# Optimization experiments

Hardware: AMD Instinct MI355X
Metric: run time of the kernel (lower is better)

## Reference

```python
import jax, jax.numpy as jnp
import numpy as np

N = 4096
FIN = 512
HID = 256
NCLS = 2
NE = 131072

def _glorot(key, fan_in, fan_out):
    r = np.sqrt(6.0 / (fan_in + fan_out))
    return jax.random.uniform(key, (fan_in, fan_out), jnp.float32, -r, r)

def setup_inputs() -> dict:
    key = jax.random.key(0)
    ks = jax.random.split(key, 16)
    X = jax.random.normal(ks[0], (N, FIN), jnp.float32)
    adj_rows = jax.random.randint(ks[1], (NE,), 0, N, jnp.int32)
    adj_cols = jax.random.randint(ks[2], (NE,), 0, N, jnp.int32)
    adj_vals = jax.random.uniform(ks[3], (NE,), jnp.float32)
    W_shared = _glorot(ks[4], FIN, HID)
    W_iv = _glorot(ks[5], HID, HID)
    W_c = _glorot(ks[6], HID, HID)
    W_r = _glorot(ks[7], HID, HID)
    Wg_iv = _glorot(ks[8], HID, HID)
    Wg_c = _glorot(ks[9], HID, HID)
    Wg_r = _glorot(ks[10], HID, HID)
    lin_W = _glorot(ks[11], 2 * HID, NCLS)
    lin_b = jnp.zeros((NCLS,), jnp.float32)
    return {"X": X, "adj_rows": adj_rows, "adj_cols": adj_cols, "adj_vals": adj_vals,
            "W_shared": W_shared, "W_iv": W_iv, "W_c": W_c, "W_r": W_r,
            "Wg_iv": Wg_iv, "Wg_c": Wg_c, "Wg_r": Wg_r, "lin_W": lin_W, "lin_b": lin_b}

def _spmm(rows, cols, vals, m):
    # sparse.mm(adj, m): out[i] = sum_{e: rows[e]==i} vals[e] * m[cols[e]]
    return jax.ops.segment_sum(vals[:, None] * m[cols], rows, num_segments=N)

def _gcn(x, rows, cols, vals, W):
    # dropout is identity in eval mode
    return jax.nn.relu(_spmm(rows, cols, vals, x @ W))

def _graphite(x, r1, r2, W):
    h = x @ W
    return jax.nn.relu(r1 @ (r1.T @ h) + r2 @ (r2.T @ h))

def reference(X, adj_rows, adj_cols, adj_vals, W_shared, W_iv, W_c, W_r, Wg_iv, Wg_c, Wg_r, lin_W, lin_b):
    h = _gcn(X, adj_rows, adj_cols, adj_vals, W_shared)
    z_iv0 = _gcn(h, adj_rows, adj_cols, adj_vals, W_iv)
    z_c0 = _gcn(h, adj_rows, adj_cols, adj_vals, W_c)
    z_r0 = _gcn(h, adj_rows, adj_cols, adj_vals, W_r)
    z_iv_rec0 = z_iv0 @ z_iv0.T
    z_c_rec0 = z_c0 @ z_c0.T
    z_r_rec0 = z_r0 @ z_r0.T
    A_dense = jnp.zeros((N, N), jnp.float32).at[adj_rows, adj_cols].add(adj_vals)
    z_iv = _graphite(z_iv0, A_dense, jax.nn.sigmoid(z_iv_rec0), Wg_iv)
    z_c = _graphite(z_c0, A_dense, jax.nn.sigmoid(z_c_rec0), Wg_c)
    z_r = _graphite(z_r0, A_dense, jax.nn.sigmoid(z_r_rec0), Wg_r)
    z_iv_rec = z_iv @ z_iv.T
    z_c_rec = z_c @ z_c.T
    z_r_rec = z_r @ z_r.T
    concat = jnp.concatenate([z_iv, z_c], axis=1)
    pred_T = jax.nn.log_softmax(concat @ lin_W + lin_b, axis=1)
    mi_total_loss = jnp.array(0.0, jnp.float32)
    return (z_iv, z_iv_rec, z_c, z_c_rec, z_r, z_r_rec, mi_total_loss, pred_T)
```

## Files before the change

kernel.cpp:

```cpp
#include <hip/hip_runtime.h>

#define Nn   4096
#define FINd 512
#define HIDd 256
#define NEd  131072

typedef unsigned short u16;
typedef __bf16 bf16x8 __attribute__((ext_vector_type(8)));
typedef float floatx4 __attribute__((ext_vector_type(4)));

__device__ __forceinline__ float bf2f(u16 u) {
  union { unsigned int i; float f; } v; v.i = ((unsigned int)u) << 16; return v.f;
}
__device__ __forceinline__ u16 f2bf(float f) {
  union { unsigned int i; float f; } v; v.f = f;
  unsigned int x = v.i;
  return (u16)((x + 0x7FFFu + ((x >> 16) & 1u)) >> 16);
}

#define GLDS(gp, lp) __builtin_amdgcn_global_load_lds( \
    (__attribute__((address_space(1))) unsigned int*)(void*)(gp), \
    (__attribute__((address_space(3))) unsigned int*)(lp), 16, 0, 0)

__global__ __launch_bounds__(256) void hist_priv_k(const int* __restrict__ rows,
                                                   const int* __restrict__ cols,
                                                   int* __restrict__ slabs) {
  __shared__ int cnt[8192];
  const int t = threadIdx.x;
  for (int i = t; i < 8192; i += 256) cnt[i] = 0;
  __syncthreads();
  int base = blockIdx.x * 4096;
  for (int i = t; i < 4096; i += 256) {
    int e = base + i;
    atomicAdd(&cnt[rows[e]], 1);
    atomicAdd(&cnt[4096 + cols[e]], 1);
  }
  __syncthreads();
  int* out = slabs + blockIdx.x * 8192;
  for (int i = t; i < 8192; i += 256) out[i] = cnt[i];
}

__global__ __launch_bounds__(1024) void scan2_k(const unsigned int* __restrict__ X,
                                                const int* __restrict__ slabs,
                                                int* __restrict__ rp, int* __restrict__ cp,
                                                int* __restrict__ rfill, int* __restrict__ cfill,
                                                int* __restrict__ flag) {
  __shared__ int part[1024];
  __shared__ int dcnt;
  const int t = threadIdx.x;
  if (t == 0) dcnt = 0;
  __syncthreads();
  int local = 0;
  for (int i = t; i < 4096; i += 1024) {
    unsigned e = (X[i] >> 7) & 0xFFu;
    if (e >= 100u && e <= 140u) local++;
  }
  if (local) atomicAdd(&dcnt, local);
  int base = t * 8, s = 0, loc[8];
  int csum[8];
#pragma unroll
  for (int j = 0; j < 8; ++j) csum[j] = 0;
  for (int sl = 0; sl < 32; ++sl) {
    const int* sp = slabs + sl * 8192 + base;
#pragma unroll
    for (int j = 0; j < 8; ++j) csum[j] += sp[j];
  }
#pragma unroll
  for (int j = 0; j < 8; ++j) { loc[j] = s; s += csum[j]; }
  part[t] = s;
  __syncthreads();
  if (t == 0) *flag = (dcnt > 2458) ? 1 : 0;
  for (int off = 1; off < 1024; off <<= 1) {
    int v = (t >= off) ? part[t - off] : 0;
    __syncthreads();
    part[t] += v;
    __syncthreads();
  }
  int excl = (t == 0) ? 0 : part[t - 1];
  int rtot = part[511];
  if (t < 512) {
#pragma unroll
    for (int j = 0; j < 8; ++j) rp[base + j] = excl + loc[j];
    if (t == 511) rp[4096] = rtot;
  } else {
    int cb = base - 4096;
    int ex2 = excl - rtot;
#pragma unroll
    for (int j = 0; j < 8; ++j) cp[cb + j] = ex2 + loc[j];
    if (t == 1023) cp[4096] = part[1023] - rtot;
  }
  for (int i = t; i < 4096; i += 1024) { rfill[i] = 0; cfill[i] = 0; }
}

__global__ __launch_bounds__(256) void setup2_k(const void* __restrict__ X,
                                                const void* __restrict__ Wsh,
                                                const void* __restrict__ W0, const void* __restrict__ W1,
                                                const void* __restrict__ W2, const void* __restrict__ G0,
                                                const void* __restrict__ G1, const void* __restrict__ G2,
                                                const void* __restrict__ linW, const void* __restrict__ linb,
                                                const int* __restrict__ rows, const int* __restrict__ cols,
                                                const void* __restrict__ vals,
                                                const int* __restrict__ rp, const int* __restrict__ cp,
                                                int* __restrict__ rfill, int* __restrict__ cfill,
                                                int2* __restrict__ rpack, int2* __restrict__ cpack,
                                                u16* __restrict__ Xb, u16* __restrict__ WshT,
                                                u16* __restrict__ WTb, u16* __restrict__ WgTb,
                                                float* __restrict__ linWf, float* __restrict__ linbf,
                                                const int* __restrict__ flag) {
  int fl = *flag;
  int bx = blockIdx.x;
  if (bx >= 10245) {
    int e = (bx - 10245) * 256 + threadIdx.x;
    if (e >= NEd) return;
    float v = fl ? bf2f(((const u16*)vals)[e]) : ((const float*)vals)[e];
    int r = rows[e], c = cols[e];
    int p1 = rp[r] + atomicAdd(&rfill[r], 1);
    rpack[p1] = make_int2(c, __float_as_int(v));
    int p2 = cp[c] + atomicAdd(&cfill[c], 1);
    cpack[p2] = make_int2(r, __float_as_int(v));
    return;
  }
  int i = bx * 256 + threadIdx.x;
  if (i < 2097152) {
    Xb[i] = fl ? ((const u16*)X)[i] : f2bf(((const float*)X)[i]);
    return;
  }
  int i2 = i - 2097152;
  if (i2 < 131072) {
    int r = i2 >> 8, c = i2 & 255;
    u16 v = fl ? ((const u16*)Wsh)[i2] : f2bf(((const float*)Wsh)[i2]);
    WshT[c * 512 + r] = v;
    return;
  }
  int i3 = i2 - 131072;
  if (i3 < 393216) {
    int w = i3 >> 16, j = i3 & 65535;
    int r = j >> 8, c = j & 255;
    const void* src = (w == 0) ? W0 : (w == 1) ? W1 : (w == 2) ? W2
                     : (w == 3) ? G0 : (w == 4) ? G1 : G2;
    u16 v = fl ? ((const u16*)src)[j] : f2bf(((const float*)src)[j]);
    u16* dst = (w < 3) ? (WTb + w * 65536) : (WgTb + (w - 3) * 65536);
    dst[c * 256 + r] = v;
    return;
  }
  int i4 = i3 - 393216;
  if (i4 < 1024) { linWf[i4] = fl ? bf2f(((const u16*)linW)[i4]) : ((const float*)linW)[i4]; return; }
  if (i4 < 1026) { int k = i4 - 1024; linbf[k] = fl ? bf2f(((const u16*)linb)[k]) : ((const float*)linb)[k]; }
}

struct SPP {
  const int* ptr; const int2* ep;
  const u16* m[3]; u16* ob[3]; unsigned long long oo[3];
};
__global__ __launch_bounds__(256) void spmm_mb_k(SPP s, const float* __restrict__ part,
                                                 void* __restrict__ outbase, int mode,
                                                 const int* __restrict__ flag) {
  const int b = blockIdx.y;
  int gid = blockIdx.x * 256 + threadIdx.x;
  int row = gid >> 6, lane = gid & 63, f = lane << 2;
  int beg = s.ptr[row], end = s.ptr[row + 1];
  const u16* m = s.m[b];
  float ax = 0.f, ay = 0.f, az = 0.f, aw = 0.f;
  int e = beg;
  for (; e + 1 < end; e += 2) {
    int2 c0 = s.ep[e];
    int2 c1 = s.ep[e + 1];
    ushort4 m0 = *(const ushort4*)(m + (size_t)c0.x * HIDd + f);
    ushort4 m1 = *(const ushort4*)(m + (size_t)c1.x * HIDd + f);
    float v0 = __int_as_float(c0.y), v1 = __int_as_float(c1.y);
    ax = fmaf(v1, bf2f(m1.x), fmaf(v0, bf2f(m0.x), ax));
    ay = fmaf(v1, bf2f(m1.y), fmaf(v0, bf2f(m0.y), ay));
    az = fmaf(v1, bf2f(m1.z), fmaf(v0, bf2f(m0.z), az));
    aw = fmaf(v1, bf2f(m1.w), fmaf(v0, bf2f(m0.w), aw));
  }
  if (e < end) {
    int2 cv = s.ep[e];
    float v = __int_as_float(cv.y);
    ushort4 mv = *(const ushort4*)(m + (size_t)cv.x * HIDd + f);
    ax = fmaf(v, bf2f(mv.x), ax);
    ay = fmaf(v, bf2f(mv.y), ay);
    az = fmaf(v, bf2f(mv.z), az);
    aw = fmaf(v, bf2f(mv.w), aw);
  }
  size_t o = (size_t)row * HIDd + f;
  if (mode == 2) {
    const float* pb = part + (size_t)b * 1048576 + o;
    float4 p0 = *(const float4*)(pb);
    float4 p1 = *(const float4*)(pb + 3145728);
    float4 p2 = *(const float4*)(pb + 2 * 3145728);
    float4 p3 = *(const float4*)(pb + 3 * 3145728);
    ax += p0.x + p1.x + p2.x + p3.x;
    ay += p0.y + p1.y + p2.y + p3.y;
    az += p0.z + p1.z + p2.z + p3.z;
    aw += p0.w + p1.w + p2.w + p3.w;
    ax = fmaxf(ax, 0.f); ay = fmaxf(ay, 0.f);
    az = fmaxf(az, 0.f); aw = fmaxf(aw, 0.f);
    ushort4 o4 = { f2bf(ax), f2bf(ay), f2bf(az), f2bf(aw) };
    *(ushort4*)(s.ob[b] + o) = o4;
    if (*flag) *(ushort4*)((u16*)outbase + s.oo[b] + o) = o4;
    else       *(float4*)((float*)outbase + s.oo[b] + o) = make_float4(ax, ay, az, aw);
  } else {
    if (mode == 0) {
      ax = fmaxf(ax, 0.f); ay = fmaxf(ay, 0.f);
      az = fmaxf(az, 0.f); aw = fmaxf(aw, 0.f);
    }
    ushort4 o4 = { f2bf(ax), f2bf(ay), f2bf(az), f2bf(aw) };
    *(ushort4*)(s.ob[b] + o) = o4;
  }
}

__global__ __launch_bounds__(256) void redt_k(const float* __restrict__ part,
                                              u16* __restrict__ tT) {
  int i = (blockIdx.x * 256 + threadIdx.x) * 4;
  float4 s0 = *(const float4*)(part + i);
  float4 s1 = *(const float4*)(part + i + 3145728);
  float4 s2 = *(const float4*)(part + i + 2 * 3145728);
  float4 s3 = *(const float4*)(part + i + 3 * 3145728);
  ushort4 o = { f2bf(s0.x + s1.x + s2.x + s3.x), f2bf(s0.y + s1.y + s2.y + s3.y),
                f2bf(s0.z + s1.z + s2.z + s3.z), f2bf(s0.w + s1.w + s2.w + s3.w) };
  *(ushort4*)(tT + i) = o;
}

struct TQ {
  const u16* Ap[3]; const u16* Bp[3]; unsigned long long c0[3];
  int tallA, K, N, kspan;
  const int* cp; const int2* cep;
  const u16* hp[3]; u16* ub[3];
};

__global__ __launch_bounds__(512) void tall_spmmu_k(TQ P, float* __restrict__ partf) {
  __shared__ __align__(16) u16 smem[24576];
  const int b = blockIdx.z;
  const int bx = blockIdx.x;
  if (bx >= 128) {
    int gid = (bx - 128) * 512 + threadIdx.x;
    int row = gid >> 6, lane = gid & 63, f = lane << 2;
    int beg = P.cp[row], end = P.cp[row + 1];
    const u16* m = P.hp[b];
    float ax = 0.f, ay = 0.f, az = 0.f, aw = 0.f;
    int e = beg;
    for (; e + 1 < end; e += 2) {
      int2 c0 = P.cep[e];
      int2 c1 = P.cep[e + 1];
      ushort4 m0 = *(const ushort4*)(m + (size_t)c0.x * HIDd + f);
      ushort4 m1 = *(const ushort4*)(m + (size_t)c1.x * HIDd + f);
      float v0 = __int_as_float(c0.y), v1 = __int_as_float(c1.y);
      ax = fmaf(v1, bf2f(m1.x), fmaf(v0, bf2f(m0.x), ax));
      ay = fmaf(v1, bf2f(m1.y), fmaf(v0, bf2f(m0.y), ay));
      az = fmaf(v1, bf2f(m1.z), fmaf(v0, bf2f(m0.z), az));
      aw = fmaf(v1, bf2f(m1.w), fmaf(v0, bf2f(m0.w), aw));
    }
    if (e < end) {
      int2 cv = P.cep[e];
      float v = __int_as_float(cv.y);
      ushort4 mv = *(const ushort4*)(m + (size_t)cv.x * HIDd + f);
      ax = fmaf(v, bf2f(mv.x), ax);
      ay = fmaf(v, bf2f(mv.y), ay);
      az = fmaf(v, bf2f(mv.z), az);
      aw = fmaf(v, bf2f(mv.w), aw);
    }
    size_t o = (size_t)row * HIDd + f;
    ushort4 o4 = { f2bf(ax), f2bf(ay), f2bf(az), f2bf(aw) };
    *(ushort4*)(P.ub[b] + o) = o4;
    return;
  }
  const u16* A = P.Ap[b];
  const u16* B = P.Bp[b];
  const int K = P.K, N = P.N, tallA = P.tallA;
  const int stripe = bx & 31, ks = bx >> 5;
  const int tid = threadIdx.x, w = tid >> 6, lane = tid & 63;
  const int lr = lane >> 3, cc = lane & 7;
  const int scol = (cc ^ lr) << 3;
  u16* As = smem;
  u16* Bs = smem + (tallA ? 16384 : 8192);
  int wrow, wcol;
  if (tallA) { wrow = (w >> 1) * 64; wcol = (w & 1) * 64; }
  else       { wrow = (w >> 2) * 64; wcol = (w & 3) * 64; }
  const int row0 = tallA ? 0 : stripe * 128;
  const int col0 = tallA ? stripe * 128 : 0;
  const int na = tallA ? 4 : 2;
  const int nb = tallA ? 2 : 4;
  floatx4 acc[4][4] = {};
  int aoff[4], boff[4];
#pragma unroll
  for (int i = 0; i < 4; ++i) {
    int m = wrow + i * 16 + (lane & 15);
    aoff[i] = m * 64 + (((lane >> 4) << 3) ^ ((m & 7) << 3));
    int n = wcol + i * 16 + (lane & 15);
    boff[i] = n * 64 + (((lane >> 4) << 3) ^ ((n & 7) << 3));
  }
  const int kbeg = ks * P.kspan, kend = kbeg + P.kspan;
  for (int k0 = kbeg; k0 < kend; k0 += 64) {
#pragma unroll
    for (int t = 0; t < 4; ++t) {
      if (t < na) {
        int ch = na * w + t;
        GLDS(A + (size_t)(row0 + 8 * ch + lr) * K + k0 + scol, As + ch * 512);
      }
      if (t < nb) {
        int ch = nb * w + t;
        GLDS(B + (size_t)(col0 + 8 * ch + lr) * K + k0 + scol, Bs + ch * 512);
      }
    }
    __syncthreads();
#pragma unroll
    for (int kk = 0; kk < 2; ++kk) {
      bf16x8 af[4], bfr[4];
#pragma unroll
      for (int i = 0; i < 4; ++i) {
        af[i]  = *(const bf16x8*)(As + (aoff[i] ^ (kk << 5)));
        bfr[i] = *(const bf16x8*)(Bs + (boff[i] ^ (kk << 5)));
      }
#pragma unroll
      for (int i = 0; i < 4; ++i)
#pragma unroll
        for (int j = 0; j < 4; ++j)
          acc[i][j] = __builtin_amdgcn_mfma_f32_16x16x32_bf16(af[i], bfr[j], acc[i][j], 0, 0, 0);
    }
    __syncthreads();
  }
  const int l15 = lane & 15, q4 = (lane >> 4) << 2;
  float* C = partf + P.c0[b] + (size_t)ks * 3145728;
  const int cbase = col0 + wcol + l15;
#pragma unroll
  for (int i = 0; i < 4; ++i)
#pragma unroll
    for (int r = 0; r < 4; ++r) {
      size_t rb = (size_t)(row0 + wrow + i * 16 + q4 + r) * N + cbase;
#pragma unroll
      for (int j = 0; j < 4; ++j) C[rb + j * 16] = acc[i][j][r];
    }
}

struct Job {
  const u16* A; const u16* B;
  const float* F1; const float* F2;
  unsigned long long c0, c1, pstride;
  int M, N, K, mode, xt, ntiles, nks, kspan, sym;
};
struct Jobs { Job j[6]; };

__global__ __launch_bounds__(256) void gemm_mega(Jobs P, void* __restrict__ WSv,
                                                 void* __restrict__ OutO,
                                                 const int* __restrict__ flag) {
  __shared__ __align__(16) u16 smem[17408];
  u16* As = smem;
  u16* Bs = smem + 8192;
  u16* Ts = smem;
  const Job jb = P.j[blockIdx.z];
  const unsigned tile = blockIdx.x;
  if ((int)tile >= jb.ntiles * jb.nks) return;
  if (jb.mode == 6) {
    int i = tile * 256 + threadIdx.x;
    const float* lw = jb.F1;
    float a0 = jb.F2[0], a1 = jb.F2[1];
    for (int f = 0; f < HIDd; ++f) {
      float zv = bf2f(jb.A[(size_t)i * HIDd + f]);
      a0 = fmaf(zv, lw[2 * f + 0], a0);
      a1 = fmaf(zv, lw[2 * f + 1], a1);
    }
    for (int f = 0; f < HIDd; ++f) {
      float zv = bf2f(jb.B[(size_t)i * HIDd + f]);
      a0 = fmaf(zv, lw[2 * (HIDd + f) + 0], a0);
      a1 = fmaf(zv, lw[2 * (HIDd + f) + 1], a1);
    }
    float mx = fmaxf(a0, a1);
    float lse = mx + logf(expf(a0 - mx) + expf(a1 - mx));
    float p0 = a0 - lse, p1 = a1 - lse;
    if (*flag) {
      u16* ob = (u16*)OutO;
      ob[jb.c0 + 2 * i + 0] = f2bf(p0);
      ob[jb.c0 + 2 * i + 1] = f2bf(p1);
      if (i == 0) ob[jb.c1] = 0;
    } else {
      float* ob = (float*)OutO;
      ob[jb.c0 + 2 * i + 0] = p0;
      ob[jb.c0 + 2 * i + 1] = p1;
      if (i == 0) ob[jb.c1] = 0.f;
    }
    return;
  }
  const unsigned ks = tile / (unsigned)jb.ntiles;
  const unsigned t2 = tile - ks * jb.ntiles;
  unsigned ty, tx;
  if (jb.sym) {
    unsigned rem = t2, rowlen = jb.xt; ty = 0;
    while (rem >= rowlen) { rem -= rowlen; --rowlen; ++ty; }
    tx = ty + rem;
  } else {
    ty = t2 / (unsigned)jb.xt;
    tx = t2 - ty * jb.xt;
  }
  const int K = jb.K, N = jb.N;
  const int row0 = ty * 128, col0 = tx * 128;
  const int tid = threadIdx.x;
  const int w = tid >> 6, lane = tid & 63;
  const int wr = (w >> 1) * 64, wc = (w & 1) * 64;
  const int lr = lane >> 3, cc = lane & 7;
  const int scol = (cc ^ lr) << 3;
  floatx4 acc[4][4] = {};
  int aoff[4], boff[4];
#pragma unroll
  for (int i = 0; i < 4; ++i) {
    int m = wr + i * 16 + (lane & 15);
    aoff[i] = m * 64 + ((((lane >> 4) << 3)) ^ ((m & 7) << 3));
    int n = wc + i * 16 + (lane & 15);
    boff[i] = n * 64 + ((((lane >> 4) << 3)) ^ ((n & 7) << 3));
  }
  const u16* A = jb.A;
  const u16* B = jb.B;
  const int kbeg = ks * jb.kspan, kend = kbeg + jb.kspan;
  for (int k0 = kbeg; k0 < kend; k0 += 64) {
#pragma unroll
    for (int t = 0; t < 4; ++t) {
      int ch = 4 * w + t;
      GLDS(A + (size_t)(row0 + 8 * ch + lr) * K + k0 + scol, As + ch * 512);
      GLDS(B + (size_t)(col0 + 8 * ch + lr) * K + k0 + scol, Bs + ch * 512);
    }
    __syncthreads();
#pragma unroll
    for (int kk = 0; kk < 2; ++kk) {
      bf16x8 af[4], bfr[4];
#pragma unroll
      for (int i = 0; i < 4; ++i) {
        af[i]  = *(const bf16x8*)(As + (aoff[i] ^ (kk << 5)));
        bfr[i] = *(const bf16x8*)(Bs + (boff[i] ^ (kk << 5)));
      }
#pragma unroll
      for (int i = 0; i < 4; ++i)
#pragma unroll
        for (int j = 0; j < 4; ++j)
          acc[i][j] = __builtin_amdgcn_mfma_f32_16x16x32_bf16(af[i], bfr[j], acc[i][j], 0, 0, 0);
    }
    __syncthreads();
  }

  const int l15 = lane & 15, q4 = (lane >> 4) << 2;
  const int cb = col0 + wc + l15;
  const int mode = jb.mode;
  if (mode == 0 || mode == 1) {
    u16* C = ((mode == 1) ? (u16*)OutO : (u16*)WSv) + jb.c0;
#pragma unroll
    for (int i = 0; i < 4; ++i)
#pragma unroll
      for (int r = 0; r < 4; ++r) {
        int lrow = wr + i * 16 + q4 + r;
        size_t rb = (size_t)(row0 + lrow) * N + cb;
#pragma unroll
        for (int j = 0; j < 4; ++j) {
          float v = acc[i][j][r];
          if (mode == 1) v = 1.f / (1.f + __expf(-v));
          u16 vb = f2bf(v);
          C[rb + j * 16] = vb;
          if (jb.sym) Ts[(wc + j * 16 + l15) * 136 + lrow] = vb;
        }
      }
    if (jb.sym && tx != ty) {
      __syncthreads();
      int rr = tid >> 1, hf = (tid & 1) << 6;
      size_t rb2 = (size_t)(col0 + rr) * N + row0 + hf;
#pragma unroll
      for (int k = 0; k < 8; ++k)
        *(uint4*)(C + rb2 + k * 8) = *(const uint4*)(Ts + rr * 136 + hf + k * 8);
    }
  } else if (mode == 4) {
    u16* C  = (u16*)WSv + jb.c0;
    u16* CT = (u16*)WSv + jb.c1;
    const int M = jb.M;
#pragma unroll
    for (int i = 0; i < 4; ++i)
#pragma unroll
      for (int r = 0; r < 4; ++r) {
        int gr = row0 + wr + i * 16 + q4 + r;
#pragma unroll
        for (int j = 0; j < 4; ++j) {
          u16 v = f2bf(acc[i][j][r]);
          int gc = cb + j * 16;
          C[(size_t)gr * N + gc] = v;
          CT[(size_t)gc * M + gr] = v;
        }
      }
  } else {
    if (*flag) {
      u16* C = (u16*)OutO + jb.c0;
#pragma unroll
      for (int i = 0; i < 4; ++i)
#pragma unroll
        for (int r = 0; r < 4; ++r) {
          int lrow = wr + i * 16 + q4 + r;
          size_t rb = (size_t)(row0 + lrow) * N + cb;
#pragma unroll
          for (int j = 0; j < 4; ++j) {
            u16 vb = f2bf(acc[i][j][r]);
            C[rb + j * 16] = vb;
            if (jb.sym) Ts[(wc + j * 16 + l15) * 136 + lrow] = vb;
          }
        }
      if (jb.sym && tx != ty) {
        __syncthreads();
        int rr = tid >> 1, hf = (tid & 1) << 6;
        size_t rb2 = (size_t)(col0 + rr) * N + row0 + hf;
#pragma unroll
        for (int k = 0; k < 8; ++k)
          *(uint4*)(C + rb2 + k * 8) = *(const uint4*)(Ts + rr * 136 + hf + k * 8);
      }
    } else {
      float* C = (float*)OutO + jb.c0;
#pragma unroll
      for (int i = 0; i < 4; ++i)
#pragma unroll
        for (int r = 0; r < 4; ++r) {
          int gr = row0 + wr + i * 16 + q4 + r;
          size_t rb = (size_t)gr * N + cb;
#pragma unroll
          for (int j = 0; j < 4; ++j) C[rb + j * 16] = acc[i][j][r];
        }
      if (jb.sym && tx != ty) {
        float* Tf = (float*)smem;
        const int whalf = w & 1;
#pragma unroll
        for (int half = 0; half < 2; ++half) {
          __syncthreads();
          if (whalf == half) {
#pragma unroll
            for (int i = 0; i < 4; ++i)
#pragma unroll
              for (int j = 0; j < 4; ++j) {
                int cl = j * 16 + l15;
#pragma unroll
                for (int r = 0; r < 4; ++r)
                  Tf[cl * 132 + wr + i * 16 + q4 + r] = acc[i][j][r];
              }
          }
          __syncthreads();
          int cl = tid >> 2, chf = (tid & 3) << 5;
          size_t rb2 = (size_t)(col0 + half * 64 + cl) * N + row0 + chf;
          const float* src = Tf + cl * 132 + chf;
#pragma unroll
          for (int k = 0; k < 8; ++k)
            *(float4*)(C + rb2 + k * 4) = *(const float4*)(src + k * 4);
        }
      }
    }
  }
}

extern "C" void kernel_launch(void* const* d_in, const int* in_sizes, int n_in,
                              void* d_out, int out_size, void* d_ws, size_t ws_size,
                              hipStream_t stream) {
  const void* X    = d_in[0];
  const int*  rows = (const int*)d_in[1];
  const int*  cols = (const int*)d_in[2];
  const void* vals = d_in[3];
  const void* Wsh  = d_in[4];

  char* W = (char*)d_ws;
  u16*  Xb    = (u16*)(W + 0);
  u16*  WshT  = (u16*)(W + 4194304);
  u16*  WTb   = (u16*)(W + 4456448);
  u16*  WgTb  = (u16*)(W + 4849664);
  int*  rp    = (int*)(W + 5242880);
  int*  cp    = (int*)(W + 5275648);
  int*  rfill = (int*)(W + 5308416);
  int*  cfill = (int*)(W + 5324800);
  int2* rpack = (int2*)(W + 5341184);
  int2* cpack = (int2*)(W + 6389760);
  float* linWf = (float*)(W + 7438336);
  float* linbf = (float*)(W + 7442432);
  int*  flag  = (int*)(W + 7442560);
  u16*  hb    = (u16*)(W + 8388608);
  u16*  tmpb[3] = { (u16*)(W + 10485760), (u16*)(W + 12582912), (u16*)(W + 14680064) };
  u16*  z0b[3]  = { (u16*)(W + 16777216), (u16*)(W + 18874368), (u16*)(W + 20971520) };
  u16*  hpb[3]  = { (u16*)(W + 23068672), (u16*)(W + 25165824), (u16*)(W + 27262976) };
  u16*  hpT[3]  = { (u16*)(W + 29360128), (u16*)(W + 31457280), (u16*)(W + 33554432) };
  u16*  tTb     = (u16*)(W + 35651584);
  u16*  zbb[3]  = { (u16*)(W + 41943040), (u16*)(W + 44040192), (u16*)(W + 46137344) };
  u16*  ubb[3]  = { (u16*)(W + 48234496), (u16*)(W + 50331648), (u16*)(W + 52428800) };
  float* partf  = (float*)(W + 54525952);
  int*  slabs  = (int*)(W + 54525952);

  const long long z_off[3]   = { 0LL, 17825792LL, 35651584LL };
  const long long rec_off[3] = { 1048576LL, 18874368LL, 36700160LL };
  const long long mi_off = 53477376LL, pred_off = 53477377LL;

  const u16* r2p[3] = { (const u16*)d_out + rec_off[0], (const u16*)d_out + rec_off[1],
                        (const u16*)d_out + rec_off[2] };

  hist_priv_k<<<32, 256, 0, stream>>>(rows, cols, slabs);
  scan2_k<<<1, 1024, 0, stream>>>((const unsigned int*)X, slabs, rp, cp, rfill, cfill, flag);
  setup2_k<<<10757, 256, 0, stream>>>(X, Wsh, d_in[5], d_in[6], d_in[7],
                                      d_in[8], d_in[9], d_in[10], d_in[11], d_in[12],
                                      rows, cols, vals, rp, cp, rfill, cfill, rpack, cpack,
                                      Xb, WshT, WTb, WgTb, linWf, linbf, flag);

  Jobs P{};
  auto setj = [](Job& j, const u16* A, const u16* B, unsigned long long c0,
                 unsigned long long c1, unsigned long long ps, int M, int N, int K,
                 int mode, int nks, int sym) {
    j.A = A; j.B = B; j.F1 = nullptr; j.F2 = nullptr;
    j.c0 = c0; j.c1 = c1; j.pstride = ps;
    j.M = M; j.N = N; j.K = K; j.mode = mode;
    j.xt = N / 128;
    j.ntiles = sym ? (j.xt * (j.xt + 1)) / 2 : (M / 128) * (N / 128);
    j.nks = nks; j.kspan = K / nks; j.sym = sym;
  };

  setj(P.j[0], Xb, WshT, ((char*)tmpb[0] - W) / 2, 0, 0, Nn, HIDd, FINd, 0, 1, 0);
  gemm_mega<<<dim3(64, 1, 1), 256, 0, stream>>>(P, d_ws, d_out, flag);

  SPP s{};
  s.ptr = rp; s.ep = rpack;
  s.m[0] = tmpb[0]; s.ob[0] = hb;
  spmm_mb_k<<<dim3(Nn / 4, 1), 256, 0, stream>>>(s, nullptr, nullptr, 0, flag);

  for (int b = 0; b < 3; ++b)
    setj(P.j[b], hb, WTb + b * 65536, ((char*)tmpb[b] - W) / 2, 0, 0, Nn, HIDd, HIDd, 0, 1, 0);
  gemm_mega<<<dim3(64, 1, 3), 256, 0, stream>>>(P, d_ws, d_out, flag);

  for (int b = 0; b < 3; ++b) { s.m[b] = tmpb[b]; s.ob[b] = z0b[b]; }
  spmm_mb_k<<<dim3(Nn / 4, 3), 256, 0, stream>>>(s, nullptr, nullptr, 0, flag);

  for (int b = 0; b < 3; ++b) {
    setj(P.j[b], z0b[b], z0b[b], rec_off[b], 0, 0, Nn, Nn, HIDd, 1, 1, 1);
    setj(P.j[3 + b], z0b[b], WgTb + b * 65536, ((char*)hpb[b] - W) / 2,
         ((char*)hpT[b] - W) / 2, 0, Nn, HIDd, HIDd, 4, 1, 0);
  }
  gemm_mega<<<dim3(528, 1, 6), 256, 0, stream>>>(P, d_ws, d_out, flag);

  TQ T{};
  for (int b = 0; b < 3; ++b) {
    T.Ap[b] = hpT[b]; T.Bp[b] = r2p[b];
    T.c0[b] = (unsigned long long)b * 1048576ULL;
    T.hp[b] = hpb[b]; T.ub[b] = ubb[b];
  }
  T.tallA = 1; T.K = Nn; T.N = Nn; T.kspan = 1024;
  T.cp = cp; T.cep = cpack;
  tall_spmmu_k<<<dim3(640, 1, 3), 512, 0, stream>>>(T, partf);

  redt_k<<<3072, 256, 0, stream>>>(partf, tTb);

  TQ T2{};
  for (int b = 0; b < 3; ++b) {
    T2.Ap[b] = r2p[b]; T2.Bp[b] = tTb + b * 1048576;
    T2.c0[b] = (unsigned long long)b * 1048576ULL;
    T2.hp[b] = nullptr; T2.ub[b] = nullptr;
  }
  T2.tallA = 0; T2.K = Nn; T2.N = HIDd; T2.kspan = 1024;
  T2.cp = nullptr; T2.cep = nullptr;
  tall_spmmu_k<<<dim3(128, 1, 3), 512, 0, stream>>>(T2, partf);

  for (int b = 0; b < 3; ++b) {
    s.m[b] = ubb[b];
    s.ob[b] = zbb[b]; s.oo[b] = (unsigned long long)z_off[b];
  }
  spmm_mb_k<<<dim3(Nn / 4, 3), 256, 0, stream>>>(s, partf, d_out, 2, flag);

  for (int b = 0; b < 3; ++b)
    setj(P.j[b], zbb[b], zbb[b], rec_off[b], 0, 0, Nn, Nn, HIDd, 3, 1, 1);
  setj(P.j[3], zbb[0], zbb[1], (unsigned long long)pred_off,
       (unsigned long long)mi_off, 0, 256, 128, 64, 6, 1, 0);
  P.j[3].ntiles = 16; P.j[3].nks = 1;
  P.j[3].F1 = linWf; P.j[3].F2 = linbf;
  gemm_mega<<<dim3(528, 1, 4), 256, 0, stream>>>(P, d_ws, d_out, flag);

  (void)in_sizes; (void)n_in; (void)out_size; (void)ws_size;
}
```

Baseline: 652.7 us.

## Overlap second-stage sparse SpMM with dense GEMM blocks, then combine separately

The final A·u sparse product is moved into spare blocks of the second tall GEMM launch, so it runs alongside the dense r2·t product instead of after it. It writes fp32 results to scratch buffers. A new lightweight combine kernel then adds the split-K partials, applies ReLU and writes the bf16 and output copies. This trades a serial SpMM stage for one extra elementwise pass over fp32 scratch, and reuses workspace regions as scratch, which must not alias live data.

```diff
diff --git a/kernel.cpp b/kernel.cpp
--- a/kernel.cpp
+++ b/kernel.cpp
@@ -152,8 +152,7 @@
   const int* ptr; const int2* ep;
   const u16* m[3]; u16* ob[3]; unsigned long long oo[3];
 };
-__global__ __launch_bounds__(256) void spmm_mb_k(SPP s, const float* __restrict__ part,
-                                                 void* __restrict__ outbase, int mode,
+__global__ __launch_bounds__(256) void spmm_mb_k(SPP s, int mode,
                                                  const int* __restrict__ flag) {
   const int b = blockIdx.y;
   int gid = blockIdx.x * 256 + threadIdx.x;
@@ -183,30 +182,37 @@
     aw = fmaf(v, bf2f(mv.w), aw);
   }
   size_t o = (size_t)row * HIDd + f;
-  if (mode == 2) {
-    const float* pb = part + (size_t)b * 1048576 + o;
-    float4 p0 = *(const float4*)(pb);
-    float4 p1 = *(const float4*)(pb + 3145728);
-    float4 p2 = *(const float4*)(pb + 2 * 3145728);
-    float4 p3 = *(const float4*)(pb + 3 * 3145728);
-    ax += p0.x + p1.x + p2.x + p3.x;
-    ay += p0.y + p1.y + p2.y + p3.y;
-    az += p0.z + p1.z + p2.z + p3.z;
-    aw += p0.w + p1.w + p2.w + p3.w;
+  if (mode == 0) {
     ax = fmaxf(ax, 0.f); ay = fmaxf(ay, 0.f);
     az = fmaxf(az, 0.f); aw = fmaxf(aw, 0.f);
-    ushort4 o4 = { f2bf(ax), f2bf(ay), f2bf(az), f2bf(aw) };
-    *(ushort4*)(s.ob[b] + o) = o4;
-    if (*flag) *(ushort4*)((u16*)outbase + s.oo[b] + o) = o4;
-    else       *(float4*)((float*)outbase + s.oo[b] + o) = make_float4(ax, ay, az, aw);
-  } else {
-    if (mode == 0) {
-      ax = fmaxf(ax, 0.f); ay = fmaxf(ay, 0.f);
-      az = fmaxf(az, 0.f); aw = fmaxf(aw, 0.f);
-    }
-    ushort4 o4 = { f2bf(ax), f2bf(ay), f2bf(az), f2bf(aw) };
-    *(ushort4*)(s.ob[b] + o) = o4;
-  }
+  }
+  ushort4 o4 = { f2bf(ax), f2bf(ay), f2bf(az), f2bf(aw) };
+  *(ushort4*)(s.ob[b] + o) = o4;
+  (void)flag;
+}
+
+struct CMB { const float* gt[3]; u16* ob[3]; unsigned long long oo[3]; };
+__global__ __launch_bounds__(256) void combine_k(CMB c, const float* __restrict__ part,
+                                                 void* __restrict__ outbase,
+                                                 const int* __restrict__ flag) {
+  const int b = blockIdx.y;
+  size_t o = ((size_t)blockIdx.x * 256 + threadIdx.x) * 4;
+  const float* pb = part + (size_t)b * 1048576 + o;
+  float4 g  = *(const float4*)(c.gt[b] + o);
+  float4 p0 = *(const float4*)(pb);
+  float4 p1 = *(const float4*)(pb + 3145728);
+  float4 p2 = *(const float4*)(pb + 2 * 3145728);
+  float4 p3 = *(const float4*)(pb + 3 * 3145728);
+  float ax = g.x + (p0.x + p1.x + p2.x + p3.x);
+  float ay = g.y + (p0.y + p1.y + p2.y + p3.y);
+  float az = g.z + (p0.z + p1.z + p2.z + p3.z);
+  float aw = g.w + (p0.w + p1.w + p2.w + p3.w);
+  ax = fmaxf(ax, 0.f); ay = fmaxf(ay, 0.f);
+  az = fmaxf(az, 0.f); aw = fmaxf(aw, 0.f);
+  ushort4 o4 = { f2bf(ax), f2bf(ay), f2bf(az), f2bf(aw) };
+  *(ushort4*)(c.ob[b] + o) = o4;
+  if (*flag) *(ushort4*)((u16*)outbase + c.oo[b] + o) = o4;
+  else       *(float4*)((float*)outbase + c.oo[b] + o) = make_float4(ax, ay, az, aw);
 }
 
 __global__ __launch_bounds__(256) void redt_k(const float* __restrict__ part,
@@ -223,9 +229,9 @@
 
 struct TQ {
   const u16* Ap[3]; const u16* Bp[3]; unsigned long long c0[3];
-  int tallA, K, N, kspan;
+  int tallA, K, N, kspan, gmode;
   const int* cp; const int2* cep;
-  const u16* hp[3]; u16* ub[3];
+  const u16* hp[3]; u16* ub[3]; float* gf[3];
 };
 
 __global__ __launch_bounds__(512) void tall_spmmu_k(TQ P, float* __restrict__ partf) {
@@ -260,8 +266,12 @@
       aw = fmaf(v, bf2f(mv.w), aw);
     }
     size_t o = (size_t)row * HIDd + f;
-    ushort4 o4 = { f2bf(ax), f2bf(ay), f2bf(az), f2bf(aw) };
-    *(ushort4*)(P.ub[b] + o) = o4;
+    if (P.gmode) {
+      *(float4*)(P.gf[b] + o) = make_float4(ax, ay, az, aw);
+    } else {
+      ushort4 o4 = { f2bf(ax), f2bf(ay), f2bf(az), f2bf(aw) };
+      *(ushort4*)(P.ub[b] + o) = o4;
+    }
     return;
   }
   const u16* A = P.Ap[b];
@@ -578,6 +588,7 @@
   u16*  ubb[3]  = { (u16*)(W + 48234496), (u16*)(W + 50331648), (u16*)(W + 52428800) };
   float* partf  = (float*)(W + 54525952);
   int*  slabs  = (int*)(W + 54525952);
+  float* gtmp[3] = { (float*)(W + 0), (float*)(W + 10485760), (float*)(W + 16777216) };
 
   const long long z_off[3]   = { 0LL, 17825792LL, 35651584LL };
   const long long rec_off[3] = { 1048576LL, 18874368LL, 36700160LL };
@@ -611,14 +622,14 @@
   SPP s{};
   s.ptr = rp; s.ep = rpack;
   s.m[0] = tmpb[0]; s.ob[0] = hb;
-  spmm_mb_k<<<dim3(Nn / 4, 1), 256, 0, stream>>>(s, nullptr, nullptr, 0, flag);
+  spmm_mb_k<<<dim3(Nn / 4, 1), 256, 0, stream>>>(s, 0, flag);
 
   for (int b = 0; b < 3; ++b)
     setj(P.j[b], hb, WTb + b * 65536, ((char*)tmpb[b] - W) / 2, 0, 0, Nn, HIDd, HIDd, 0, 1, 0);
   gemm_mega<<<dim3(64, 1, 3), 256, 0, stream>>>(P, d_ws, d_out, flag);
 
   for (int b = 0; b < 3; ++b) { s.m[b] = tmpb[b]; s.ob[b] = z0b[b]; }
-  spmm_mb_k<<<dim3(Nn / 4, 3), 256, 0, stream>>>(s, nullptr, nullptr, 0, flag);
+  spmm_mb_k<<<dim3(Nn / 4, 3), 256, 0, stream>>>(s, 0, flag);
 
   for (int b = 0; b < 3; ++b) {
     setj(P.j[b], z0b[b], z0b[b], rec_off[b], 0, 0, Nn, Nn, HIDd, 1, 1, 1);
@@ -631,9 +642,9 @@
   for (int b = 0; b < 3; ++b) {
     T.Ap[b] = hpT[b]; T.Bp[b] = r2p[b];
     T.c0[b] = (unsigned long long)b * 1048576ULL;
-    T.hp[b] = hpb[b]; T.ub[b] = ubb[b];
-  }
-  T.tallA = 1; T.K = Nn; T.N = Nn; T.kspan = 1024;
+    T.hp[b] = hpb[b]; T.ub[b] = ubb[b]; T.gf[b] = nullptr;
+  }
+  T.tallA = 1; T.K = Nn; T.N = Nn; T.kspan = 1024; T.gmode = 0;
   T.cp = cp; T.cep = cpack;
   tall_spmmu_k<<<dim3(640, 1, 3), 512, 0, stream>>>(T, partf);
 
@@ -643,17 +654,18 @@
   for (int b = 0; b < 3; ++b) {
     T2.Ap[b] = r2p[b]; T2.Bp[b] = tTb + b * 1048576;
     T2.c0[b] = (unsigned long long)b * 1048576ULL;
-    T2.hp[b] = nullptr; T2.ub[b] = nullptr;
-  }
-  T2.tallA = 0; T2.K = Nn; T2.N = HIDd; T2.kspan = 1024;
-  T2.cp = nullptr; T2.cep = nullptr;
-  tall_spmmu_k<<<dim3(128, 1, 3), 512, 0, stream>>>(T2, partf);
-
+    T2.hp[b] = ubb[b]; T2.ub[b] = nullptr; T2.gf[b] = gtmp[b];
+  }
+  T2.tallA = 0; T2.K = Nn; T2.N = HIDd; T2.kspan = 1024; T2.gmode = 1;
+  T2.cp = rp; T2.cep = rpack;
+  tall_spmmu_k<<<dim3(640, 1, 3), 512, 0, stream>>>(T2, partf);
+
+  CMB cmb{};
   for (int b = 0; b < 3; ++b) {
-    s.m[b] = ubb[b];
-    s.ob[b] = zbb[b]; s.oo[b] = (unsigned long long)z_off[b];
-  }
-  spmm_mb_k<<<dim3(Nn / 4, 3), 256, 0, stream>>>(s, partf, d_out, 2, flag);
+    cmb.gt[b] = gtmp[b];
+    cmb.ob[b] = zbb[b]; cmb.oo[b] = (unsigned long long)z_off[b];
+  }
+  combine_k<<<dim3(1024, 3), 256, 0, stream>>>(cmb, partf, d_out, flag);
 
   for (int b = 0; b < 3; ++b)
     setj(P.j[b], zbb[b], zbb[b], rec_off[b], 0, 0, Nn, Nn, HIDd, 3, 1, 1);
```

After: 676.2 us. +3.6%, slower.
